# Performance work log

Measured on AMD Instinct MI355X. Metric: run time of the kernel, lower is better.

The kernel has to match this reference:

```python
import jax, jax.numpy as jnp
import numpy as np

N_NODES = 50000
N_EDGES = 800000
IN_FEAT = 256
DIM_H = 64
DIM_OUT = 64


def setup_inputs() -> dict:
    key = jax.random.key(0)
    ks = jax.random.split(key, 9)
    x = jax.random.normal(ks[0], (N_NODES, IN_FEAT), dtype=jnp.float32)
    edge_index = jax.random.randint(ks[1], (2, N_EDGES), 0, N_NODES, dtype=jnp.int64)
    s_in = 1.0 / np.sqrt(IN_FEAT)
    s_h = 1.0 / np.sqrt(DIM_H)
    W_src = jax.random.normal(ks[2], (IN_FEAT, DIM_H), dtype=jnp.float32) * s_in
    W_dst = jax.random.normal(ks[3], (IN_FEAT, DIM_H), dtype=jnp.float32) * s_in
    att_src = jax.random.normal(ks[4], (DIM_H,), dtype=jnp.float32) * s_h
    att_dst = jax.random.normal(ks[5], (DIM_H,), dtype=jnp.float32) * s_h
    bias_conv = jax.random.normal(ks[6], (DIM_H,), dtype=jnp.float32) * 0.01
    W_lin = jax.random.normal(ks[7], (DIM_H, DIM_OUT), dtype=jnp.float32) * s_h
    b_lin = jax.random.normal(ks[8], (DIM_OUT,), dtype=jnp.float32) * 0.01
    return {"x": x, "edge_index": edge_index, "W_src": W_src, "W_dst": W_dst,
            "att_src": att_src, "att_dst": att_dst, "bias_conv": bias_conv,
            "W_lin": W_lin, "b_lin": b_lin}


def reference(x, edge_index, W_src, W_dst, att_src, att_dst, bias_conv, W_lin, b_lin):
    N = x.shape[0]
    src, dst = edge_index[0], edge_index[1]
    # linear projections (GATConv lin_src / lin_dst, no bias)
    h_src = x @ W_src                      # [N, H]
    h_dst = x @ W_dst                      # [N, H]
    # per-node attention logits
    a_src = h_src @ att_src                # [N]
    a_dst = h_dst @ att_dst                # [N]
    # edge-wise score: leaky_relu(a_src[src] + a_dst[dst])
    e = jax.nn.leaky_relu(a_src[src] + a_dst[dst], negative_slope=0.2)  # [E]
    # segment softmax over destination neighborhoods
    e_max = jax.ops.segment_max(e, dst, num_segments=N)
    e_exp = jnp.exp(e - e_max[dst])
    denom = jax.ops.segment_sum(e_exp, dst, num_segments=N)
    alpha = e_exp / denom[dst]             # [E]
    # weighted scatter-add aggregation
    msg = h_src[src] * alpha[:, None]      # [E, H]
    out = jax.ops.segment_sum(msg, dst, num_segments=N) + bias_conv  # [N, H]
    h = jax.nn.relu(out)
    return h @ W_lin + b_lin               # [N, dim_out]
```

## Files before the change

kernel.cpp:

```cpp
#include <hip/hip_runtime.h>
#include <math.h>

#define N_NODES 50000
#define N_EDGES 800000
#define IN_FEAT 256
#define DIM_H   64
#define NPAD    50176
#define CAP     48
#define NBUK2   1568
#define BCAP2   768
#define EPB     4096
#define PBLKS   784
#define ABLKS   196
#define PNODES  32

typedef __attribute__((ext_vector_type(8)))  short  s16x8;
typedef __attribute__((ext_vector_type(16))) float  f32x16;

__device__ __forceinline__ float bcast_f(float v, int k) {
  return __int_as_float(__builtin_amdgcn_readlane(__float_as_int(v), k));
}
__device__ __forceinline__ short f2bf(float f) {
  unsigned u = __float_as_uint(f);
  u += 0x7fffu + ((u >> 16) & 1u);
  return (short)(u >> 16);
}

__global__ __launch_bounds__(256) void prep_kernel(
    const float* __restrict__ Wsrc,
    const float* __restrict__ Wdst,
    const float* __restrict__ att_dst,
    float* __restrict__ wdl_g,
    short* __restrict__ wfrag_g,
    int* __restrict__ gbc) {
  __shared__ float attl[DIM_H];
  const int tid = threadIdx.x;

  for (int i = tid; i < 2048; i += 256) gbc[i] = 0;

  if (tid < DIM_H) attl[tid] = att_dst[tid];
  __syncthreads();

  {
    float s = 0.f;
    const float4* row = (const float4*)(Wdst + (long)tid * DIM_H);
    #pragma unroll
    for (int q = 0; q < 16; ++q) {
      float4 r = row[q];
      s = fmaf(r.x, attl[4 * q + 0], s);
      s = fmaf(r.y, attl[4 * q + 1], s);
      s = fmaf(r.z, attl[4 * q + 2], s);
      s = fmaf(r.w, attl[4 * q + 3], s);
    }
    wdl_g[tid] = s;
  }

  for (int e4 = tid * 4; e4 < IN_FEAT * DIM_H; e4 += 1024) {
    float4 w4 = *(const float4*)(Wsrc + e4);
    int k = e4 >> 6, n0 = e4 & 63;
    int sg = k >> 4, half = (k >> 3) & 1, j = k & 7, t = n0 >> 5;
    short* p = &wfrag_g[((sg * 2 + t) * 64 + ((n0 & 31) + 32 * half)) * 8 + j];
    p[0]  = f2bf(w4.x);
    p[8]  = f2bf(w4.y);
    p[16] = f2bf(w4.z);
    p[24] = f2bf(w4.w);
  }
}

__global__ __launch_bounds__(256, 4) void proj_binA_kernel(
    const float* __restrict__ x,
    const float* __restrict__ wdl_g,
    const short* __restrict__ wfrag_g,
    const float* __restrict__ att_src,
    const int* __restrict__ ei,
    unsigned* __restrict__ hbf,
    float* __restrict__ a_src,
    float* __restrict__ a_dst,
    int* __restrict__ gbc,
    unsigned* __restrict__ binbuf) {
  __shared__ short wfrag[16 * 2 * 64 * 8];
  __shared__ float wdl[IN_FEAT];

  const int tid = threadIdx.x;

  if (blockIdx.x >= PBLKS) {
    int* bcnt = (int*)wfrag;
    int* wcur = bcnt + NBUK2;
    const int e0 = (blockIdx.x - PBLKS) * EPB;

    for (int b = tid; b < NBUK2; b += 256) bcnt[b] = 0;
    __syncthreads();

    int dst[16];
    #pragma unroll
    for (int i = 0; i < 16; ++i) {
      int e = e0 + tid + 256 * i;
      dst[i] = (e < N_EDGES) ? ei[N_EDGES + e] : -1;
      if (dst[i] >= 0) atomicAdd(&bcnt[dst[i] >> 5], 1);
    }
    __syncthreads();

    for (int b = tid; b < NBUK2; b += 256) {
      int c = bcnt[b];
      wcur[b] = c ? atomicAdd(&gbc[b], c) : 0;
    }
    __syncthreads();

    #pragma unroll
    for (int i = 0; i < 16; ++i) {
      int e = e0 + tid + 256 * i;
      if (e < N_EDGES) {
        int s = ei[e];
        int b = dst[i] >> 5;
        int pos = atomicAdd(&wcur[b], 1);
        if (pos < BCAP2)
          binbuf[(long)b * BCAP2 + pos] =
              (unsigned)s | ((unsigned)(dst[i] & 31) << 16);
      }
    }
    return;
  }

  const int lane = tid & 63;
  const int wv   = tid >> 6;
  const int tile = wv >> 1;
  const int h    = wv & 1;

  if (tid < 64) ((float4*)wdl)[tid] = ((const float4*)wdl_g)[tid];
  {
    uint4* d = (uint4*)wfrag;
    const uint4* s4 = (const uint4*)wfrag_g;
    for (int i = tid; i < 2048; i += 256) d[i] = s4[i];
  }
  __syncthreads();

  const int base  = blockIdx.x * 64 + tile * 32;
  int row = base + (lane & 31); if (row > N_NODES - 1) row = N_NODES - 1;
  const int koff8 = (lane >> 5) * 8;
  const int k0    = h * 128;
  const float* px = x + (long)row * IN_FEAT + k0 + koff8;

  f32x16 acc0, acc1;
  #pragma unroll
  for (int i = 0; i < 16; ++i) { acc0[i] = 0.f; acc1[i] = 0.f; }
  float pd = 0.f;

  #pragma unroll
  for (int s = 0; s < 8; ++s) {
    float4 va = *(const float4*)(px + s * 16);
    float4 vb = *(const float4*)(px + s * 16 + 4);
    const float* wp = wdl + k0 + s * 16 + koff8;
    float4 w1 = *(const float4*)(wp);
    float4 w2 = *(const float4*)(wp + 4);
    pd = fmaf(va.x, w1.x, pd); pd = fmaf(va.y, w1.y, pd);
    pd = fmaf(va.z, w1.z, pd); pd = fmaf(va.w, w1.w, pd);
    pd = fmaf(vb.x, w2.x, pd); pd = fmaf(vb.y, w2.y, pd);
    pd = fmaf(vb.z, w2.z, pd); pd = fmaf(vb.w, w2.w, pd);
    s16x8 a;
    a[0] = f2bf(va.x); a[1] = f2bf(va.y); a[2] = f2bf(va.z); a[3] = f2bf(va.w);
    a[4] = f2bf(vb.x); a[5] = f2bf(vb.y); a[6] = f2bf(vb.z); a[7] = f2bf(vb.w);
    const int f = (h * 8 + s) * 2;
    s16x8 b0 = *(const s16x8*)(wfrag + ((f + 0) * 64 + lane) * 8);
    s16x8 b1 = *(const s16x8*)(wfrag + ((f + 1) * 64 + lane) * 8);
    acc0 = __builtin_amdgcn_mfma_f32_32x32x16_bf16(a, b0, acc0, 0, 0, 0);
    acc1 = __builtin_amdgcn_mfma_f32_32x32x16_bf16(a, b1, acc1, 0, 0, 0);
  }
  float pds = pd + __shfl_xor(pd, 32, 64);

  __syncthreads();
  float* fa = (float*)wfrag;
  float* myslot = fa + tile * 2304 + lane * 36;
  float* pdb    = fa + 4608 + tile * 32;

  if (h == 1) {
    #pragma unroll
    for (int i = 0; i < 4; ++i)
      *(float4*)(myslot + i * 4) =
          make_float4(acc0[4 * i], acc0[4 * i + 1], acc0[4 * i + 2], acc0[4 * i + 3]);
    #pragma unroll
    for (int i = 0; i < 4; ++i)
      *(float4*)(myslot + 16 + i * 4) =
          make_float4(acc1[4 * i], acc1[4 * i + 1], acc1[4 * i + 2], acc1[4 * i + 3]);
    if (lane < 32) pdb[lane] = pds;
  }
  __syncthreads();
  if (h == 1) return;

  #pragma unroll
  for (int i = 0; i < 4; ++i) {
    float4 t = *(const float4*)(myslot + i * 4);
    acc0[4 * i] += t.x; acc0[4 * i + 1] += t.y;
    acc0[4 * i + 2] += t.z; acc0[4 * i + 3] += t.w;
  }
  #pragma unroll
  for (int i = 0; i < 4; ++i) {
    float4 t = *(const float4*)(myslot + 16 + i * 4);
    acc1[4 * i] += t.x; acc1[4 * i + 1] += t.y;
    acc1[4 * i + 2] += t.z; acc1[4 * i + 3] += t.w;
  }
  pds += pdb[lane & 31];

  const int col = lane & 31;
  const int rhi = 4 * (lane >> 5);

  #pragma unroll
  for (int r = 0; r < 16; ++r) {
    int node = base + (r & 3) + 8 * (r >> 2) + rhi;
    if (node < N_NODES) {
      unsigned p = (unsigned)(unsigned short)f2bf(acc0[r]) |
                   ((unsigned)(unsigned short)f2bf(acc1[r]) << 16);
      hbf[(long)node * 32 + col] = p;
    }
  }

  float att0 = att_src[col];
  float att1 = att_src[col + 32];
  #pragma unroll
  for (int r = 0; r < 16; ++r) {
    float t = acc0[r] * att0 + acc1[r] * att1;
    t += __shfl_xor(t, 1, 64);
    t += __shfl_xor(t, 2, 64);
    t += __shfl_xor(t, 4, 64);
    t += __shfl_xor(t, 8, 64);
    t += __shfl_xor(t, 16, 64);
    int node = base + (r & 3) + 8 * (r >> 2) + rhi;
    if (col == 0 && node < N_NODES) a_src[node] = t;
  }

  int node = base + (lane & 31);
  if (lane < 32 && node < N_NODES) a_dst[node] = pds;
}

__global__ __launch_bounds__(256) void gatherfused_kernel(
    const unsigned* __restrict__ binbuf,
    const int* __restrict__ gbc,
    const float* __restrict__ a_src,
    const float* __restrict__ a_dst,
    const unsigned* __restrict__ hbf,
    const float* __restrict__ bias_conv,
    const float* __restrict__ W_lin,
    const float* __restrict__ b_lin,
    float* __restrict__ out) {
  __shared__ unsigned rec[PNODES * CAP];
  __shared__ int   lcnt[PNODES];
  __shared__ float adl[PNODES];
  __shared__ float wl[64 * 64];

  const int tid    = threadIdx.x;
  const int bucket = blockIdx.x;
  const int nb     = bucket * PNODES;

  {
    const float4* wsrc4 = (const float4*)W_lin;
    float4* wl4 = (float4*)wl;
    for (int i = tid; i < 1024; i += 256) wl4[i] = wsrc4[i];
  }
  if (tid < PNODES) {
    lcnt[tid] = 0;
    adl[tid]  = a_dst[nb + tid];
  }
  __syncthreads();

  int count = gbc[bucket]; if (count > BCAP2) count = BCAP2;
  const unsigned* bb = binbuf + (long)bucket * BCAP2;
  for (int i = tid; i < count; i += 256) {
    unsigned u = bb[i];
    int dl = (int)(u >> 16);
    int s  = (int)(u & 0xffffu);
    float sc = a_src[s] + adl[dl];
    sc = sc >= 0.f ? sc : 0.2f * sc;
    float w = __expf(sc);
    int pos = atomicAdd(&lcnt[dl], 1);
    if (pos < CAP)
      rec[dl * CAP + pos] =
          ((unsigned)(unsigned short)f2bf(w) << 16) | (u & 0xffffu);
  }
  __syncthreads();

  const int lane = tid & 63;
  const int wv   = __builtin_amdgcn_readfirstlane(tid >> 6);
  const int grp8 = lane >> 3;
  const int ql8  = lane & 7;
  const float bj  = bias_conv[lane];
  const float blj = b_lin[lane];

  auto prefetch = [&](int dl, int m_, float& W0, float& W1, uint4& HP0, uint4& HP1) {
    if (m_ > 0) {
      int i0 = (grp8     < m_) ? grp8     : m_ - 1;
      int i1 = (8 + grp8 < m_) ? 8 + grp8 : m_ - 1;
      unsigned u0 = rec[dl * CAP + i0];
      unsigned u1 = rec[dl * CAP + i1];
      W0 = (grp8     < m_) ? __uint_as_float(u0 & 0xffff0000u) : 0.f;
      W1 = (8 + grp8 < m_) ? __uint_as_float(u1 & 0xffff0000u) : 0.f;
      HP0 = *(const uint4*)(hbf + (long)(u0 & 0xffffu) * 32 + ql8 * 4);
      HP1 = *(const uint4*)(hbf + (long)(u1 & 0xffffu) * 32 + ql8 * 4);
    } else {
      W0 = 0.f; W1 = 0.f;
      HP0 = make_uint4(0u, 0u, 0u, 0u);
      HP1 = make_uint4(0u, 0u, 0u, 0u);
    }
  };

  int mcur = lcnt[wv * 8]; if (mcur > CAP) mcur = CAP;
  float pw0, pw1; uint4 php0, php1;
  prefetch(wv * 8, mcur, pw0, pw1, php0, php1);

  #pragma unroll
  for (int q = 0; q < 8; ++q) {
    const int dl = wv * 8 + q;
    const int n  = nb + dl;
    const int m  = mcur;

    float alo[4] = {0.f, 0.f, 0.f, 0.f};
    float ahi[4] = {0.f, 0.f, 0.f, 0.f};
    float den = 0.f;

    {
      alo[0] = fmaf(pw0, __uint_as_float(php0.x << 16),         alo[0]);
      ahi[0] = fmaf(pw0, __uint_as_float(php0.x & 0xffff0000u), ahi[0]);
      alo[1] = fmaf(pw0, __uint_as_float(php0.y << 16),         alo[1]);
      ahi[1] = fmaf(pw0, __uint_as_float(php0.y & 0xffff0000u), ahi[1]);
      alo[2] = fmaf(pw0, __uint_as_float(php0.z << 16),         alo[2]);
      ahi[2] = fmaf(pw0, __uint_as_float(php0.z & 0xffff0000u), ahi[2]);
      alo[3] = fmaf(pw0, __uint_as_float(php0.w << 16),         alo[3]);
      ahi[3] = fmaf(pw0, __uint_as_float(php0.w & 0xffff0000u), ahi[3]);
      den += pw0;
      alo[0] = fmaf(pw1, __uint_as_float(php1.x << 16),         alo[0]);
      ahi[0] = fmaf(pw1, __uint_as_float(php1.x & 0xffff0000u), ahi[0]);
      alo[1] = fmaf(pw1, __uint_as_float(php1.y << 16),         alo[1]);
      ahi[1] = fmaf(pw1, __uint_as_float(php1.y & 0xffff0000u), ahi[1]);
      alo[2] = fmaf(pw1, __uint_as_float(php1.z << 16),         alo[2]);
      ahi[2] = fmaf(pw1, __uint_as_float(php1.z & 0xffff0000u), ahi[2]);
      alo[3] = fmaf(pw1, __uint_as_float(php1.w << 16),         alo[3]);
      ahi[3] = fmaf(pw1, __uint_as_float(php1.w & 0xffff0000u), ahi[3]);
      den += pw1;
    }

    if (q < 7) {
      mcur = lcnt[dl + 1]; if (mcur > CAP) mcur = CAP;
      prefetch(dl + 1, mcur, pw0, pw1, php0, php1);
    }

    for (int j = 16; j < m; j += 16) {
      int idx0 = j + grp8;
      int idx1 = j + 8 + grp8;
      int ci0 = idx0 < m ? idx0 : m - 1;
      int ci1 = idx1 < m ? idx1 : m - 1;
      unsigned u0 = rec[dl * CAP + ci0];
      unsigned u1 = rec[dl * CAP + ci1];
      float w0 = __uint_as_float(u0 & 0xffff0000u);
      float w1 = __uint_as_float(u1 & 0xffff0000u);
      if (idx0 >= m) w0 = 0.f;
      if (idx1 >= m) w1 = 0.f;
      int s0 = (int)(u0 & 0xffffu);
      int s1 = (int)(u1 & 0xffffu);
      uint4 hp0 = *(const uint4*)(hbf + (long)s0 * 32 + ql8 * 4);
      uint4 hp1 = *(const uint4*)(hbf + (long)s1 * 32 + ql8 * 4);
      alo[0] = fmaf(w0, __uint_as_float(hp0.x << 16),         alo[0]);
      ahi[0] = fmaf(w0, __uint_as_float(hp0.x & 0xffff0000u), ahi[0]);
      alo[1] = fmaf(w0, __uint_as_float(hp0.y << 16),         alo[1]);
      ahi[1] = fmaf(w0, __uint_as_float(hp0.y & 0xffff0000u), ahi[1]);
      alo[2] = fmaf(w0, __uint_as_float(hp0.z << 16),         alo[2]);
      ahi[2] = fmaf(w0, __uint_as_float(hp0.z & 0xffff0000u), ahi[2]);
      alo[3] = fmaf(w0, __uint_as_float(hp0.w << 16),         alo[3]);
      ahi[3] = fmaf(w0, __uint_as_float(hp0.w & 0xffff0000u), ahi[3]);
      den += w0;
      alo[0] = fmaf(w1, __uint_as_float(hp1.x << 16),         alo[0]);
      ahi[0] = fmaf(w1, __uint_as_float(hp1.x & 0xffff0000u), ahi[0]);
      alo[1] = fmaf(w1, __uint_as_float(hp1.y << 16),         alo[1]);
      ahi[1] = fmaf(w1, __uint_as_float(hp1.y & 0xffff0000u), ahi[1]);
      alo[2] = fmaf(w1, __uint_as_float(hp1.z << 16),         alo[2]);
      ahi[2] = fmaf(w1, __uint_as_float(hp1.z & 0xffff0000u), ahi[2]);
      alo[3] = fmaf(w1, __uint_as_float(hp1.w << 16),         alo[3]);
      ahi[3] = fmaf(w1, __uint_as_float(hp1.w & 0xffff0000u), ahi[3]);
      den += w1;
    }

    #pragma unroll
    for (int mm = 8; mm <= 32; mm <<= 1) {
      #pragma unroll
      for (int c = 0; c < 4; ++c) {
        alo[c] += __shfl_xor(alo[c], mm, 64);
        ahi[c] += __shfl_xor(ahi[c], mm, 64);
      }
      den += __shfl_xor(den, mm, 64);
    }
    int srcl = (lane & 31) >> 2;
    float v0 = __shfl(alo[0], srcl, 64);
    float v1 = __shfl(alo[1], srcl, 64);
    float v2 = __shfl(alo[2], srcl, 64);
    float v3 = __shfl(alo[3], srcl, 64);
    float v4 = __shfl(ahi[0], srcl, 64);
    float v5 = __shfl(ahi[1], srcl, 64);
    float v6 = __shfl(ahi[2], srcl, 64);
    float v7 = __shfl(ahi[3], srcl, 64);
    int c4 = lane & 3;
    float losel = (c4 == 0) ? v0 : (c4 == 1) ? v1 : (c4 == 2) ? v2 : v3;
    float hisel = (c4 == 0) ? v4 : (c4 == 1) ? v5 : (c4 == 2) ? v6 : v7;
    float accl = (lane >> 5) ? hisel : losel;

    float inv = den > 0.f ? 1.0f / den : 0.f;
    float z = fmaf(accl, inv, bj);
    float hh = fmaxf(z, 0.f);
    float o0 = blj, o1 = 0.f, o2 = 0.f, o3 = 0.f;
    #pragma unroll
    for (int k = 0; k < 64; k += 4) {
      o0 = fmaf(bcast_f(hh, k + 0), wl[(k + 0) * 64 + lane], o0);
      o1 = fmaf(bcast_f(hh, k + 1), wl[(k + 1) * 64 + lane], o1);
      o2 = fmaf(bcast_f(hh, k + 2), wl[(k + 2) * 64 + lane], o2);
      o3 = fmaf(bcast_f(hh, k + 3), wl[(k + 3) * 64 + lane], o3);
    }
    float o = (o0 + o1) + (o2 + o3);
    if (n < N_NODES) out[(long)n * DIM_H + lane] = o;
  }
}

extern "C" void kernel_launch(void* const* d_in, const int* in_sizes, int n_in,
                              void* d_out, int out_size, void* d_ws, size_t ws_size,
                              hipStream_t stream) {
  const float* x        = (const float*)d_in[0];
  const int*   ei       = (const int*)d_in[1];
  const float* Wsrc     = (const float*)d_in[2];
  const float* Wdst     = (const float*)d_in[3];
  const float* att_src  = (const float*)d_in[4];
  const float* att_dst  = (const float*)d_in[5];
  const float* bias_cv  = (const float*)d_in[6];
  const float* W_lin    = (const float*)d_in[7];
  const float* b_lin    = (const float*)d_in[8];
  float* out = (float*)d_out;

  unsigned* hbf    = (unsigned*)d_ws;
  float*    a_src  = (float*)(hbf + 1600000);
  float*    a_dst  = a_src + NPAD;
  int*      gbc    = (int*)(a_dst + NPAD);
  unsigned* binbuf = (unsigned*)(gbc + 2048);
  float*    wdl_g  = (float*)(binbuf + (long)NBUK2 * BCAP2);
  short*    wfrag_g = (short*)(wdl_g + 256);

  prep_kernel<<<1, 256, 0, stream>>>(Wsrc, Wdst, att_dst, wdl_g, wfrag_g, gbc);

  proj_binA_kernel<<<PBLKS + ABLKS, 256, 0, stream>>>(
      x, wdl_g, wfrag_g, att_src, ei, hbf, a_src, a_dst, gbc, binbuf);

  gatherfused_kernel<<<NBUK2, 256, 0, stream>>>(
      binbuf, gbc, a_src, a_dst, hbf, bias_cv, W_lin, b_lin, out);
}
```

Measured before the change: 176.9 us.

## Fold weight prep into projection kernel and use MFMA for output linear

Removes the single-block prep kernel: each projection block now computes Wdst·att_dst and the bf16 MFMA fragment of W_src itself, and the bucket counters are cleared with a memset. In the gather kernel, the per-node readlane-based 64x64 output GEMV is replaced by staging relu'd hidden rows in shared memory and running a bf16 32x32x16 MFMA per bucket on two waves. This aims to cut a serial launch and the scalar output matmul, but repeats the weight conversion in every one of the 784 blocks and adds bf16 rounding on the final linear.

```diff
diff --git a/kernel.cpp b/kernel.cpp
--- a/kernel.cpp
+++ b/kernel.cpp
@@ -17,61 +17,18 @@
 typedef __attribute__((ext_vector_type(8)))  short  s16x8;
 typedef __attribute__((ext_vector_type(16))) float  f32x16;
 
-__device__ __forceinline__ float bcast_f(float v, int k) {
-  return __int_as_float(__builtin_amdgcn_readlane(__float_as_int(v), k));
-}
 __device__ __forceinline__ short f2bf(float f) {
   unsigned u = __float_as_uint(f);
   u += 0x7fffu + ((u >> 16) & 1u);
   return (short)(u >> 16);
 }
 
-__global__ __launch_bounds__(256) void prep_kernel(
+__global__ __launch_bounds__(256, 4) void proj_binA_kernel(
+    const float* __restrict__ x,
     const float* __restrict__ Wsrc,
     const float* __restrict__ Wdst,
+    const float* __restrict__ att_src,
     const float* __restrict__ att_dst,
-    float* __restrict__ wdl_g,
-    short* __restrict__ wfrag_g,
-    int* __restrict__ gbc) {
-  __shared__ float attl[DIM_H];
-  const int tid = threadIdx.x;
-
-  for (int i = tid; i < 2048; i += 256) gbc[i] = 0;
-
-  if (tid < DIM_H) attl[tid] = att_dst[tid];
-  __syncthreads();
-
-  {
-    float s = 0.f;
-    const float4* row = (const float4*)(Wdst + (long)tid * DIM_H);
-    #pragma unroll
-    for (int q = 0; q < 16; ++q) {
-      float4 r = row[q];
-      s = fmaf(r.x, attl[4 * q + 0], s);
-      s = fmaf(r.y, attl[4 * q + 1], s);
-      s = fmaf(r.z, attl[4 * q + 2], s);
-      s = fmaf(r.w, attl[4 * q + 3], s);
-    }
-    wdl_g[tid] = s;
-  }
-
-  for (int e4 = tid * 4; e4 < IN_FEAT * DIM_H; e4 += 1024) {
-    float4 w4 = *(const float4*)(Wsrc + e4);
-    int k = e4 >> 6, n0 = e4 & 63;
-    int sg = k >> 4, half = (k >> 3) & 1, j = k & 7, t = n0 >> 5;
-    short* p = &wfrag_g[((sg * 2 + t) * 64 + ((n0 & 31) + 32 * half)) * 8 + j];
-    p[0]  = f2bf(w4.x);
-    p[8]  = f2bf(w4.y);
-    p[16] = f2bf(w4.z);
-    p[24] = f2bf(w4.w);
-  }
-}
-
-__global__ __launch_bounds__(256, 4) void proj_binA_kernel(
-    const float* __restrict__ x,
-    const float* __restrict__ wdl_g,
-    const short* __restrict__ wfrag_g,
-    const float* __restrict__ att_src,
     const int* __restrict__ ei,
     unsigned* __restrict__ hbf,
     float* __restrict__ a_src,
@@ -80,6 +37,7 @@
     unsigned* __restrict__ binbuf) {
   __shared__ short wfrag[16 * 2 * 64 * 8];
   __shared__ float wdl[IN_FEAT];
+  __shared__ float attl[DIM_H];
 
   const int tid = threadIdx.x;
 
@@ -126,11 +84,32 @@
   const int tile = wv >> 1;
   const int h    = wv & 1;
 
-  if (tid < 64) ((float4*)wdl)[tid] = ((const float4*)wdl_g)[tid];
+  if (tid < DIM_H) attl[tid] = att_dst[tid];
+  __syncthreads();
+
   {
-    uint4* d = (uint4*)wfrag;
-    const uint4* s4 = (const uint4*)wfrag_g;
-    for (int i = tid; i < 2048; i += 256) d[i] = s4[i];
+    float s = 0.f;
+    const float4* row = (const float4*)(Wdst + (long)tid * DIM_H);
+    #pragma unroll
+    for (int q = 0; q < 16; ++q) {
+      float4 r = row[q];
+      s = fmaf(r.x, attl[4 * q + 0], s);
+      s = fmaf(r.y, attl[4 * q + 1], s);
+      s = fmaf(r.z, attl[4 * q + 2], s);
+      s = fmaf(r.w, attl[4 * q + 3], s);
+    }
+    wdl[tid] = s;
+  }
+
+  for (int e4 = tid * 4; e4 < IN_FEAT * DIM_H; e4 += 1024) {
+    float4 w4 = *(const float4*)(Wsrc + e4);
+    int k = e4 >> 6, n0 = e4 & 63;
+    int s = k >> 4, half = (k >> 3) & 1, j = k & 7, t = n0 >> 5;
+    short* p = &wfrag[((s * 2 + t) * 64 + ((n0 & 31) + 32 * half)) * 8 + j];
+    p[0]  = f2bf(w4.x);
+    p[8]  = f2bf(w4.y);
+    p[16] = f2bf(w4.z);
+    p[24] = f2bf(w4.w);
   }
   __syncthreads();
 
@@ -244,16 +223,22 @@
   __shared__ unsigned rec[PNODES * CAP];
   __shared__ int   lcnt[PNODES];
   __shared__ float adl[PNODES];
-  __shared__ float wl[64 * 64];
+  __shared__ short wlf[4096];
+  __shared__ float hl[PNODES * 68];
 
   const int tid    = threadIdx.x;
   const int bucket = blockIdx.x;
   const int nb     = bucket * PNODES;
 
-  {
-    const float4* wsrc4 = (const float4*)W_lin;
-    float4* wl4 = (float4*)wl;
-    for (int i = tid; i < 1024; i += 256) wl4[i] = wsrc4[i];
+  for (int e4 = tid * 4; e4 < DIM_H * DIM_H; e4 += 1024) {
+    float4 w4 = *(const float4*)(W_lin + e4);
+    int k = e4 >> 6, n0 = e4 & 63;
+    int s = k >> 4, half = (k >> 3) & 1, j = k & 7, t = n0 >> 5;
+    short* p = &wlf[((s * 2 + t) * 64 + ((n0 & 31) + 32 * half)) * 8 + j];
+    p[0]  = f2bf(w4.x);
+    p[8]  = f2bf(w4.y);
+    p[16] = f2bf(w4.z);
+    p[24] = f2bf(w4.w);
   }
   if (tid < PNODES) {
     lcnt[tid] = 0;
@@ -281,8 +266,13 @@
   const int wv   = __builtin_amdgcn_readfirstlane(tid >> 6);
   const int grp8 = lane >> 3;
   const int ql8  = lane & 7;
-  const float bj  = bias_conv[lane];
-  const float blj = b_lin[lane];
+
+  float bcl[4], bch[4];
+  #pragma unroll
+  for (int c = 0; c < 4; ++c) {
+    bcl[c] = bias_conv[ql8 * 4 + c];
+    bch[c] = bias_conv[32 + ql8 * 4 + c];
+  }
 
   auto prefetch = [&](int dl, int m_, float& W0, float& W1, uint4& HP0, uint4& HP1) {
     if (m_ > 0) {
@@ -308,7 +298,6 @@
   #pragma unroll
   for (int q = 0; q < 8; ++q) {
     const int dl = wv * 8 + q;
-    const int n  = nb + dl;
     const int m  = mcur;
 
     float alo[4] = {0.f, 0.f, 0.f, 0.f};
@@ -385,33 +374,49 @@
       }
       den += __shfl_xor(den, mm, 64);
     }
-    int srcl = (lane & 31) >> 2;
-    float v0 = __shfl(alo[0], srcl, 64);
-    float v1 = __shfl(alo[1], srcl, 64);
-    float v2 = __shfl(alo[2], srcl, 64);
-    float v3 = __shfl(alo[3], srcl, 64);
-    float v4 = __shfl(ahi[0], srcl, 64);
-    float v5 = __shfl(ahi[1], srcl, 64);
-    float v6 = __shfl(ahi[2], srcl, 64);
-    float v7 = __shfl(ahi[3], srcl, 64);
-    int c4 = lane & 3;
-    float losel = (c4 == 0) ? v0 : (c4 == 1) ? v1 : (c4 == 2) ? v2 : v3;
-    float hisel = (c4 == 0) ? v4 : (c4 == 1) ? v5 : (c4 == 2) ? v6 : v7;
-    float accl = (lane >> 5) ? hisel : losel;
-
-    float inv = den > 0.f ? 1.0f / den : 0.f;
-    float z = fmaf(accl, inv, bj);
-    float hh = fmaxf(z, 0.f);
-    float o0 = blj, o1 = 0.f, o2 = 0.f, o3 = 0.f;
-    #pragma unroll
-    for (int k = 0; k < 64; k += 4) {
-      o0 = fmaf(bcast_f(hh, k + 0), wl[(k + 0) * 64 + lane], o0);
-      o1 = fmaf(bcast_f(hh, k + 1), wl[(k + 1) * 64 + lane], o1);
-      o2 = fmaf(bcast_f(hh, k + 2), wl[(k + 2) * 64 + lane], o2);
-      o3 = fmaf(bcast_f(hh, k + 3), wl[(k + 3) * 64 + lane], o3);
-    }
-    float o = (o0 + o1) + (o2 + o3);
-    if (n < N_NODES) out[(long)n * DIM_H + lane] = o;
+
+    if (grp8 == 0) {
+      float inv = den > 0.f ? 1.0f / den : 0.f;
+      float4 hlo, hhi;
+      hlo.x = fmaxf(fmaf(alo[0], inv, bcl[0]), 0.f);
+      hlo.y = fmaxf(fmaf(alo[1], inv, bcl[1]), 0.f);
+      hlo.z = fmaxf(fmaf(alo[2], inv, bcl[2]), 0.f);
+      hlo.w = fmaxf(fmaf(alo[3], inv, bcl[3]), 0.f);
+      hhi.x = fmaxf(fmaf(ahi[0], inv, bch[0]), 0.f);
+      hhi.y = fmaxf(fmaf(ahi[1], inv, bch[1]), 0.f);
+      hhi.z = fmaxf(fmaf(ahi[2], inv, bch[2]), 0.f);
+      hhi.w = fmaxf(fmaf(ahi[3], inv, bch[3]), 0.f);
+      *(float4*)(&hl[dl * 68 + ql8 * 4])      = hlo;
+      *(float4*)(&hl[dl * 68 + 32 + ql8 * 4]) = hhi;
+    }
+  }
+  __syncthreads();
+
+  if (wv < 2) {
+    f32x16 acc;
+    #pragma unroll
+    for (int i = 0; i < 16; ++i) acc[i] = 0.f;
+    const int mrow  = lane & 31;
+    const int khalf = (lane >> 5) * 8;
+    #pragma unroll
+    for (int s = 0; s < 4; ++s) {
+      float4 va = *(const float4*)(&hl[mrow * 68 + s * 16 + khalf]);
+      float4 vb = *(const float4*)(&hl[mrow * 68 + s * 16 + khalf + 4]);
+      s16x8 a;
+      a[0] = f2bf(va.x); a[1] = f2bf(va.y); a[2] = f2bf(va.z); a[3] = f2bf(va.w);
+      a[4] = f2bf(vb.x); a[5] = f2bf(vb.y); a[6] = f2bf(vb.z); a[7] = f2bf(vb.w);
+      s16x8 b = *(const s16x8*)(wlf + ((s * 2 + wv) * 64 + lane) * 8);
+      acc = __builtin_amdgcn_mfma_f32_32x32x16_bf16(a, b, acc, 0, 0, 0);
+    }
+    const int col  = (lane & 31) + 32 * wv;
+    const float blv = b_lin[col];
+    const int rbase = 4 * (lane >> 5);
+    #pragma unroll
+    for (int r = 0; r < 16; ++r) {
+      int row = (r & 3) + 8 * (r >> 2) + rbase;
+      int n = nb + row;
+      if (n < N_NODES) out[(long)n * DIM_H + col] = acc[r] + blv;
+    }
   }
 }
 
@@ -434,13 +439,11 @@
   float*    a_dst  = a_src + NPAD;
   int*      gbc    = (int*)(a_dst + NPAD);
   unsigned* binbuf = (unsigned*)(gbc + 2048);
-  float*    wdl_g  = (float*)(binbuf + (long)NBUK2 * BCAP2);
-  short*    wfrag_g = (short*)(wdl_g + 256);
-
-  prep_kernel<<<1, 256, 0, stream>>>(Wsrc, Wdst, att_dst, wdl_g, wfrag_g, gbc);
+
+  hipMemsetAsync(gbc, 0, 2048 * sizeof(int), stream);
 
   proj_binA_kernel<<<PBLKS + ABLKS, 256, 0, stream>>>(
-      x, wdl_g, wfrag_g, att_src, ei, hbf, a_src, a_dst, gbc, binbuf);
+      x, Wsrc, Wdst, att_src, att_dst, ei, hbf, a_src, a_dst, gbc, binbuf);
 
   gatherfused_kernel<<<NBUK2, 256, 0, stream>>>(
       binbuf, gbc, a_src, a_dst, hbf, bias_cv, W_lin, b_lin, out);
```

Measured after the change: 159.8 us. 9.7% less time.
